# Kernel tuning notes

Measured on AMD Instinct MI355X. Metric: run time of the kernel, lower is better.

## Reference

```python
import jax, jax.numpy as jnp
import numpy as np

NUM_NODES = 116
EMBED = 64
HIDDEN = 64
OUT_FEAT = 116


def mish(x):
    return x * jnp.tanh(jax.nn.softplus(x))


def sage_conv(x, src, dst, w_l, b_l, w_r, n):
    # PyG SAGEConv (mean aggr): out = lin_l(mean_{j->i} x_j) + lin_r(x_i)
    agg = jax.ops.segment_sum(x[src], dst, num_segments=n)
    cnt = jax.ops.segment_sum(jnp.ones((src.shape[0],), x.dtype), dst, num_segments=n)
    mean = agg / jnp.clip(cnt, 1.0)[:, None]
    return mean @ w_l.T + b_l + x @ w_r.T


def setup_inputs() -> dict:
    key = jax.random.key(0)
    ks = jax.random.split(key, 12)
    B = 64
    N = B * NUM_NODES          # 7424 total nodes
    E = N * 32                 # 237568 edges
    d_in = EMBED * NUM_NODES   # 7424
    d_hid = HIDDEN * NUM_NODES # 7424
    d_out = OUT_FEAT * NUM_NODES  # 13456

    def lin_w(k, fan_out, fan_in):
        s = 1.0 / np.sqrt(fan_in)
        return jax.random.uniform(k, (fan_out, fan_in), jnp.float32, -s, s)

    return {
        "z": jax.random.normal(ks[0], (N, EMBED), jnp.float32),
        "edge_index": jax.random.randint(ks[1], (2, E), 0, N, jnp.int64),
        "batch_size": B,
        "w1_l": lin_w(ks[2], EMBED, EMBED),
        "b1_l": jnp.zeros((EMBED,), jnp.float32),
        "w1_r": lin_w(ks[3], EMBED, EMBED),
        "w2_l": lin_w(ks[4], EMBED, EMBED),
        "b2_l": jnp.zeros((EMBED,), jnp.float32),
        "w2_r": lin_w(ks[5], EMBED, EMBED),
        "fc1_w": lin_w(ks[6], d_hid, d_in),
        "fc1_b": jax.random.uniform(ks[7], (d_hid,), jnp.float32, -1/np.sqrt(d_in), 1/np.sqrt(d_in)),
        "fc2_w": lin_w(ks[8], d_out, d_hid),
        "fc2_b": jax.random.uniform(ks[9], (d_out,), jnp.float32, -1/np.sqrt(d_hid), 1/np.sqrt(d_hid)),
    }


def reference(z, edge_index, batch_size, w1_l, b1_l, w1_r, w2_l, b2_l, w2_r,
              fc1_w, fc1_b, fc2_w, fc2_b):
    n = z.shape[0]
    src, dst = edge_index[0], edge_index[1]
    h = mish(sage_conv(z, src, dst, w1_l, b1_l, w1_r, n))
    h = mish(sage_conv(h, src, dst, w2_l, b2_l, w2_r, n))
    h_flat = h.reshape(batch_size, NUM_NODES * EMBED)
    hidden = mish(h_flat @ fc1_w.T + fc1_b)
    x_rec = (hidden @ fc2_w.T + fc2_b).reshape(batch_size, NUM_NODES, OUT_FEAT)
    # enforce symmetry, unit diagonal
    sym = 0.5 * (x_rec + jnp.swapaxes(x_rec, 1, 2))
    eye = jnp.eye(NUM_NODES, dtype=bool)[None]
    sym = jnp.where(eye, jnp.asarray(1.0, sym.dtype), sym)
    return sym.reshape(batch_size * NUM_NODES, OUT_FEAT)
```

## Files before the change

kernel.cpp:

```cpp
#include <hip/hip_runtime.h>
#include <math.h>

#define NODES_TOT 7424
#define EDGES     237568
#define BATCH     64
#define NN        116
#define KDIM      7424
#define N1        7424
#define N2        13456
#define NKB       116
#define KSPLIT    8

typedef __attribute__((ext_vector_type(8))) short bf16x8;
typedef __attribute__((ext_vector_type(4))) float f32x4;
typedef __attribute__((ext_vector_type(4))) short s16x4;

__device__ __forceinline__ float mish_f(float v) {
    float sp = fmaxf(v, 0.0f) + log1pf(expf(-fabsf(v)));
    return v * tanhf(sp);
}

__device__ __forceinline__ unsigned short bf_rne(float f) {
    unsigned u = __float_as_uint(f);
    u += 0x7fffu + ((u >> 16) & 1u);
    return (unsigned short)(u >> 16);
}

__global__ void zero_kernel(int* __restrict__ p, int n) {
    int i = blockIdx.x * 256 + threadIdx.x;
    if (i < n) p[i] = 0;
}

__global__ void hist_kernel(const int* __restrict__ dst, int* __restrict__ hist) {
    int e = blockIdx.x * 256 + threadIdx.x;
    if (e < EDGES) atomicAdd(&hist[dst[e]], 1);
}

__global__ void scan_kernel(const int* __restrict__ hist, int* __restrict__ row_start,
                            int* __restrict__ cursor) {
    __shared__ int s[1024];
    int t = threadIdx.x;
    int base = t * 8;
    int loc[8];
    int sum = 0;
    #pragma unroll
    for (int c = 0; c < 8; ++c) {
        int idx = base + c;
        int v = (idx < NODES_TOT) ? hist[idx] : 0;
        loc[c] = sum;
        sum += v;
    }
    s[t] = sum;
    __syncthreads();
    for (int off = 1; off < 1024; off <<= 1) {
        int v = (t >= off) ? s[t - off] : 0;
        __syncthreads();
        s[t] += v;
        __syncthreads();
    }
    int excl = s[t] - sum;
    #pragma unroll
    for (int c = 0; c < 8; ++c) {
        int idx = base + c;
        if (idx < NODES_TOT) {
            int r = excl + loc[c];
            row_start[idx] = r;
            cursor[idx] = r;
        }
    }
}

__global__ void csr_fill_kernel(const int* __restrict__ src, const int* __restrict__ dst,
                                int* __restrict__ cursor, int* __restrict__ csr_src) {
    int e = blockIdx.x * 256 + threadIdx.x;
    if (e < EDGES) {
        int p = atomicAdd(&cursor[dst[e]], 1);
        csr_src[p] = src[e];
    }
}

template <bool BF>
__global__ void __launch_bounds__(256) conv_kernel(
        const float* __restrict__ x, const int* __restrict__ csr_src,
        const int* __restrict__ row_start, const int* __restrict__ deg_arr,
        const float* __restrict__ w_l, const float* __restrict__ b_l,
        const float* __restrict__ w_r, void* __restrict__ h_out_v) {
    __shared__ float wlT[64 * 64];
    __shared__ float wrT[64 * 64];
    __shared__ float mv[4][64];
    __shared__ float xv[4][64];
    int t = threadIdx.x;
    for (int i = 0; i < 16; ++i) {
        int idx = t + i * 256;
        int f = idx >> 6, k = idx & 63;
        wlT[k * 64 + f] = w_l[idx];
        wrT[k * 64 + f] = w_r[idx];
    }
    int g = t >> 6, f = t & 63;
    __syncthreads();
    for (int nb = blockIdx.x * 4; nb < NODES_TOT; nb += gridDim.x * 4) {
        int node = nb + g;
        int deg = deg_arr[node];
        int rs = row_start[node];
        float sum = 0.f;
        for (int e = 0; e < deg; ++e) {
            int s = csr_src[rs + e];
            sum += x[s * 64 + f];
        }
        float mean = sum / (float)max(deg, 1);
        mv[g][f] = mean;
        xv[g][f] = x[node * 64 + f];
        __syncthreads();
        float o = b_l[f];
        #pragma unroll
        for (int k = 0; k < 64; ++k) {
            o = fmaf(mv[g][k], wlT[k * 64 + f], o);
            o = fmaf(xv[g][k], wrT[k * 64 + f], o);
        }
        float m = mish_f(o);
        if (BF) ((unsigned short*)h_out_v)[node * 64 + f] = bf_rne(m);
        else    ((float*)h_out_v)[node * 64 + f] = m;
        __syncthreads();
    }
}

template <int KSHIFT>
__global__ void __launch_bounds__(256) gemm_tile(
        const unsigned short* __restrict__ Abf, const float* __restrict__ W,
        float* __restrict__ Cp, int N) {
    __shared__ __align__(16) short Wsh[2][4096];
    __shared__ __align__(16) short Ash[2][4096];
    int t = threadIdx.x;
    int bx = blockIdx.x, by = blockIdx.y;
    int kb0 = (by * NKB) >> KSHIFT;
    int kb1 = ((by + 1) * NKB) >> KSHIFT;
    int S = kb1 - kb0;
    int n0 = bx * 64;
    int r = t >> 2, q = t & 3;
    int wr = n0 + r; if (wr >= N) wr = N - 1;
    const float*          wsrc = W   + (size_t)wr * KDIM + (size_t)kb0 * 64 + q * 4;
    const unsigned short* asrc = Abf + (size_t)r  * KDIM + (size_t)kb0 * 64 + q * 8;
    int fb = q >> 1, hf = q & 1;
    int wv = t >> 6, l = t & 63, l15 = l & 15, hi = l >> 4;
    f32x4 acc[4];
    #pragma unroll
    for (int g = 0; g < 4; ++g) acc[g] = (f32x4){0.f, 0.f, 0.f, 0.f};

    f32x4 wA0, wA1, wA2, wA3, wB0, wB1, wB2, wB3;
    bf16x8 aA0, aA1, aB0, aB1;

#define ISSUE(W0, W1, W2, W3, A0, A1, step) do {                          \
        size_t kk = (size_t)(step) * 64;                                  \
        W0 = *(const f32x4*)(wsrc + kk);                                  \
        W1 = *(const f32x4*)(wsrc + kk + 16);                             \
        W2 = *(const f32x4*)(wsrc + kk + 32);                             \
        W3 = *(const f32x4*)(wsrc + kk + 48);                             \
        A0 = *(const bf16x8*)(asrc + kk);                                 \
        A1 = *(const bf16x8*)(asrc + kk + 32);                            \
    } while (0)

#define CONVWRITE(W0, W1, W2, W3, A0, A1, b) do {                         \
        s16x4 cv0, cv1, cv2, cv3;                                         \
        _Pragma("unroll")                                                 \
        for (int j = 0; j < 4; ++j) {                                     \
            cv0[j] = (short)bf_rne(W0[j]);                                \
            cv1[j] = (short)bf_rne(W1[j]);                                \
            cv2[j] = (short)bf_rne(W2[j]);                                \
            cv3[j] = (short)bf_rne(W3[j]);                                \
        }                                                                 \
        *(s16x4*)&Wsh[b][((0 * 2 + fb) * 64 + r) * 8 + hf * 4] = cv0;     \
        *(s16x4*)&Wsh[b][((1 * 2 + fb) * 64 + r) * 8 + hf * 4] = cv1;     \
        *(s16x4*)&Wsh[b][((2 * 2 + fb) * 64 + r) * 8 + hf * 4] = cv2;     \
        *(s16x4*)&Wsh[b][((3 * 2 + fb) * 64 + r) * 8 + hf * 4] = cv3;     \
        *(bf16x8*)&Ash[b][(q * 64 + r) * 8] = A0;                         \
        *(bf16x8*)&Ash[b][((q + 4) * 64 + r) * 8] = A1;                   \
    } while (0)

#define MFMAPH(b) do {                                                    \
        _Pragma("unroll")                                                 \
        for (int s = 0; s < 2; ++s) {                                     \
            int fw = s * 4 + hi;                                          \
            bf16x8 bh = *(const bf16x8*)&Wsh[b][(fw * 64 + wv * 16 + l15) * 8]; \
            _Pragma("unroll")                                             \
            for (int g = 0; g < 4; ++g) {                                 \
                bf16x8 av = *(const bf16x8*)&Ash[b][(fw * 64 + g * 16 + l15) * 8]; \
                acc[g] = __builtin_amdgcn_mfma_f32_16x16x32_bf16(av, bh, acc[g], 0, 0, 0); \
            }                                                             \
        }                                                                 \
    } while (0)

#define BAR() asm volatile("s_waitcnt lgkmcnt(0)\n\ts_barrier" ::: "memory")

    ISSUE(wA0, wA1, wA2, wA3, aA0, aA1, 0);
    ISSUE(wB0, wB1, wB2, wB3, aB0, aB1, 1);
    CONVWRITE(wA0, wA1, wA2, wA3, aA0, aA1, 0);
    BAR();

    int i = 0;
    for (; i + 1 < S - 1; i += 2) {
        if (i + 2 < S) ISSUE(wA0, wA1, wA2, wA3, aA0, aA1, i + 2);
        MFMAPH(0);
        CONVWRITE(wB0, wB1, wB2, wB3, aB0, aB1, 1);
        BAR();
        if (i + 3 < S) ISSUE(wB0, wB1, wB2, wB3, aB0, aB1, i + 3);
        MFMAPH(1);
        CONVWRITE(wA0, wA1, wA2, wA3, aA0, aA1, 0);
        BAR();
    }
    if (i < S - 1) {
        MFMAPH(0);
        CONVWRITE(wB0, wB1, wB2, wB3, aB0, aB1, 1);
        BAR();
        MFMAPH(1);
    } else {
        MFMAPH(0);
    }

#undef ISSUE
#undef CONVWRITE
#undef MFMAPH
#undef BAR

    int gn = n0 + wv * 16 + l15;
    if (gn < N) {
        float* cp = Cp + (size_t)by * 64 * N;
        #pragma unroll
        for (int g = 0; g < 4; ++g)
            #pragma unroll
            for (int rr = 0; rr < 4; ++rr)
                cp[(size_t)(g * 16 + hi * 4 + rr) * N + gn] = acc[g][rr];
    }
}

__global__ void reduce1_kernel(const float* __restrict__ Cp, const float* __restrict__ b,
                               unsigned short* __restrict__ A2) {
    int i4 = (blockIdx.x * 256 + threadIdx.x) * 4;
    if (i4 >= BATCH * N1) return;
    int n = i4 % N1;
    f32x4 acc = *(const f32x4*)(b + n);
    #pragma unroll
    for (int s = 0; s < KSPLIT; ++s)
        acc += *(const f32x4*)(Cp + (size_t)s * BATCH * N1 + i4);
    s16x4 o;
    #pragma unroll
    for (int j = 0; j < 4; ++j) o[j] = (short)bf_rne(mish_f(acc[j]));
    *(s16x4*)(A2 + i4) = o;
}

__global__ void reduce2_kernel(const float* __restrict__ Cp, const float* __restrict__ b,
                               float* __restrict__ C2) {
    int i4 = (blockIdx.x * 256 + threadIdx.x) * 4;
    if (i4 >= BATCH * N2) return;
    int n = i4 % N2;
    f32x4 acc = *(const f32x4*)(b + n);
    #pragma unroll
    for (int s = 0; s < KSPLIT; ++s)
        acc += *(const f32x4*)(Cp + (size_t)s * BATCH * N2 + i4);
    *(f32x4*)(C2 + i4) = acc;
}

__global__ void sym_kernel(const float* __restrict__ C2, float* __restrict__ out) {
    int tid = blockIdx.x * 256 + threadIdx.x;
    if (tid >= BATCH * NN * NN) return;
    int j = tid % NN;
    int r = tid / NN;
    int i = r % NN;
    int b = r / NN;
    float v;
    if (i == j) {
        v = 1.0f;
    } else {
        v = 0.5f * (C2[(size_t)b * N2 + i * NN + j] + C2[(size_t)b * N2 + j * NN + i]);
    }
    out[tid] = v;
}

extern "C" void kernel_launch(void* const* d_in, const int* in_sizes, int n_in,
                              void* d_out, int out_size, void* d_ws, size_t ws_size,
                              hipStream_t stream) {
    const float* z     = (const float*)d_in[0];
    const int*   edge  = (const int*)d_in[1];
    const float* w1_l  = (const float*)d_in[3];
    const float* b1_l  = (const float*)d_in[4];
    const float* w1_r  = (const float*)d_in[5];
    const float* w2_l  = (const float*)d_in[6];
    const float* b2_l  = (const float*)d_in[7];
    const float* w2_r  = (const float*)d_in[8];
    const float* fc1_w = (const float*)d_in[9];
    const float* fc1_b = (const float*)d_in[10];
    const float* fc2_w = (const float*)d_in[11];
    const float* fc2_b = (const float*)d_in[12];
    float* out = (float*)d_out;

    char* ws = (char*)d_ws;
    size_t off = 0;
    auto alloc = [&](size_t bytes) {
        void* p = ws + off;
        off = (off + bytes + 255) & ~(size_t)255;
        return p;
    };
    int*            hist      = (int*)alloc(NODES_TOT * 4);
    int*            row_start = (int*)alloc(NODES_TOT * 4);
    int*            cursor    = (int*)alloc(NODES_TOT * 4);
    int*            csr_src   = (int*)alloc((size_t)EDGES * 4);
    float*          h1        = (float*)alloc((size_t)NODES_TOT * 64 * 4);
    unsigned short* A1        = (unsigned short*)alloc((size_t)NODES_TOT * 64 * 2);
    float*          Cp1       = (float*)alloc((size_t)KSPLIT * BATCH * N1 * 4);
    unsigned short* A2        = (unsigned short*)alloc((size_t)BATCH * N1 * 2);
    float*          Cp2       = (float*)alloc((size_t)KSPLIT * BATCH * N2 * 4);
    float*          C2        = (float*)alloc((size_t)BATCH * N2 * 4);

    const int* src = edge;
    const int* dst = edge + EDGES;

    zero_kernel<<<(NODES_TOT + 255) / 256, 256, 0, stream>>>(hist, NODES_TOT);
    hist_kernel<<<(EDGES + 255) / 256, 256, 0, stream>>>(dst, hist);
    scan_kernel<<<1, 1024, 0, stream>>>(hist, row_start, cursor);
    csr_fill_kernel<<<(EDGES + 255) / 256, 256, 0, stream>>>(src, dst, cursor, csr_src);

    conv_kernel<false><<<928, 256, 0, stream>>>(z, csr_src, row_start, hist, w1_l, b1_l, w1_r, h1);
    conv_kernel<true><<<928, 256, 0, stream>>>(h1, csr_src, row_start, hist, w2_l, b2_l, w2_r, A1);

    gemm_tile<3><<<dim3(N1 / 64, KSPLIT), 256, 0, stream>>>(A1, fc1_w, Cp1, N1);
    reduce1_kernel<<<(BATCH * N1 / 4 + 255) / 256, 256, 0, stream>>>(Cp1, fc1_b, A2);

    gemm_tile<3><<<dim3((N2 + 63) / 64, KSPLIT), 256, 0, stream>>>(A2, fc2_w, Cp2, N2);
    reduce2_kernel<<<(BATCH * N2 / 4 + 255) / 256, 256, 0, stream>>>(Cp2, fc2_b, C2);

    sym_kernel<<<(BATCH * NN * NN + 255) / 256, 256, 0, stream>>>(C2, out);
}
```

Measured before the change: 324.4 us.

## Halve GEMM K-split and load weight rows in two-step bursts

The split-K factor for both FC GEMMs drops from 8 to 4, and each block now walks a fixed 29 k-blocks. Weight loads are issued in 128-element bursts covering two k-steps, so each thread issues wider contiguous reads further ahead of the MFMA phases. This halves the partial-sum traffic written and reduced, but launches half as many blocks and holds more loaded data in registers. The result could be lower occupancy or too few blocks to keep the GPU's compute units busy.

```diff
diff --git a/kernel.cpp b/kernel.cpp
--- a/kernel.cpp
+++ b/kernel.cpp
@@ -8,8 +8,7 @@
 #define KDIM      7424
 #define N1        7424
 #define N2        13456
-#define NKB       116
-#define KSPLIT    8
+#define KSPLIT    4
 
 typedef __attribute__((ext_vector_type(8))) short bf16x8;
 typedef __attribute__((ext_vector_type(4))) float f32x4;
@@ -124,42 +123,51 @@
     }
 }
 
-template <int KSHIFT>
-__global__ void __launch_bounds__(256) gemm_tile(
+__global__ void __launch_bounds__(256) gemm_burst(
         const unsigned short* __restrict__ Abf, const float* __restrict__ W,
         float* __restrict__ Cp, int N) {
     __shared__ __align__(16) short Wsh[2][4096];
     __shared__ __align__(16) short Ash[2][4096];
     int t = threadIdx.x;
     int bx = blockIdx.x, by = blockIdx.y;
-    int kb0 = (by * NKB) >> KSHIFT;
-    int kb1 = ((by + 1) * NKB) >> KSHIFT;
-    int S = kb1 - kb0;
     int n0 = bx * 64;
     int r = t >> 2, q = t & 3;
     int wr = n0 + r; if (wr >= N) wr = N - 1;
-    const float*          wsrc = W   + (size_t)wr * KDIM + (size_t)kb0 * 64 + q * 4;
-    const unsigned short* asrc = Abf + (size_t)r  * KDIM + (size_t)kb0 * 64 + q * 8;
+    const float*          wsrc = W   + (size_t)wr * KDIM + (size_t)by * 29 * 64 + q * 4;
+    const unsigned short* asrc = Abf + (size_t)r  * KDIM + (size_t)by * 29 * 64 + q * 8;
     int fb = q >> 1, hf = q & 1;
     int wv = t >> 6, l = t & 63, l15 = l & 15, hi = l >> 4;
     f32x4 acc[4];
     #pragma unroll
     for (int g = 0; g < 4; ++g) acc[g] = (f32x4){0.f, 0.f, 0.f, 0.f};
 
-    f32x4 wA0, wA1, wA2, wA3, wB0, wB1, wB2, wB3;
-    bf16x8 aA0, aA1, aB0, aB1;
-
-#define ISSUE(W0, W1, W2, W3, A0, A1, step) do {                          \
-        size_t kk = (size_t)(step) * 64;                                  \
-        W0 = *(const f32x4*)(wsrc + kk);                                  \
-        W1 = *(const f32x4*)(wsrc + kk + 16);                             \
-        W2 = *(const f32x4*)(wsrc + kk + 32);                             \
-        W3 = *(const f32x4*)(wsrc + kk + 48);                             \
-        A0 = *(const bf16x8*)(asrc + kk);                                 \
-        A1 = *(const bf16x8*)(asrc + kk + 32);                            \
-    } while (0)
-
-#define CONVWRITE(W0, W1, W2, W3, A0, A1, b) do {                         \
+    f32x4 wA[8], wB[8];
+    bf16x8 aEv[2], aOd[2];
+
+#define IW2(dst, s) do {                                                  \
+        dst[0] = *(const f32x4*)(wsrc + (s) * 64 + 0);                    \
+        dst[1] = *(const f32x4*)(wsrc + (s) * 64 + 16);                   \
+        dst[2] = *(const f32x4*)(wsrc + (s) * 64 + 32);                   \
+        dst[3] = *(const f32x4*)(wsrc + (s) * 64 + 48);                   \
+        dst[4] = *(const f32x4*)(wsrc + (s) * 64 + 64);                   \
+        dst[5] = *(const f32x4*)(wsrc + (s) * 64 + 80);                   \
+        dst[6] = *(const f32x4*)(wsrc + (s) * 64 + 96);                   \
+        dst[7] = *(const f32x4*)(wsrc + (s) * 64 + 112);                  \
+    } while (0)
+
+#define IW1(dst, s) do {                                                  \
+        dst[0] = *(const f32x4*)(wsrc + (s) * 64 + 0);                    \
+        dst[1] = *(const f32x4*)(wsrc + (s) * 64 + 16);                   \
+        dst[2] = *(const f32x4*)(wsrc + (s) * 64 + 32);                   \
+        dst[3] = *(const f32x4*)(wsrc + (s) * 64 + 48);                   \
+    } while (0)
+
+#define IA(dst, s) do {                                                   \
+        dst[0] = *(const bf16x8*)(asrc + (s) * 64);                       \
+        dst[1] = *(const bf16x8*)(asrc + (s) * 64 + 32);                  \
+    } while (0)
+
+#define CW(W0, W1, W2, W3, av, b) do {                                    \
         s16x4 cv0, cv1, cv2, cv3;                                         \
         _Pragma("unroll")                                                 \
         for (int j = 0; j < 4; ++j) {                                     \
@@ -168,12 +176,12 @@
             cv2[j] = (short)bf_rne(W2[j]);                                \
             cv3[j] = (short)bf_rne(W3[j]);                                \
         }                                                                 \
-        *(s16x4*)&Wsh[b][((0 * 2 + fb) * 64 + r) * 8 + hf * 4] = cv0;     \
-        *(s16x4*)&Wsh[b][((1 * 2 + fb) * 64 + r) * 8 + hf * 4] = cv1;     \
-        *(s16x4*)&Wsh[b][((2 * 2 + fb) * 64 + r) * 8 + hf * 4] = cv2;     \
-        *(s16x4*)&Wsh[b][((3 * 2 + fb) * 64 + r) * 8 + hf * 4] = cv3;     \
-        *(bf16x8*)&Ash[b][(q * 64 + r) * 8] = A0;                         \
-        *(bf16x8*)&Ash[b][((q + 4) * 64 + r) * 8] = A1;                   \
+        *(s16x4*)&Wsh[b][((0 + fb) * 64 + r) * 8 + hf * 4] = cv0;         \
+        *(s16x4*)&Wsh[b][((2 + fb) * 64 + r) * 8 + hf * 4] = cv1;         \
+        *(s16x4*)&Wsh[b][((4 + fb) * 64 + r) * 8 + hf * 4] = cv2;         \
+        *(s16x4*)&Wsh[b][((6 + fb) * 64 + r) * 8 + hf * 4] = cv3;         \
+        *(bf16x8*)&Ash[b][(q * 64 + r) * 8] = av[0];                      \
+        *(bf16x8*)&Ash[b][((q + 4) * 64 + r) * 8] = av[1];                \
     } while (0)
 
 #define MFMAPH(b) do {                                                    \
@@ -183,43 +191,50 @@
             bf16x8 bh = *(const bf16x8*)&Wsh[b][(fw * 64 + wv * 16 + l15) * 8]; \
             _Pragma("unroll")                                             \
             for (int g = 0; g < 4; ++g) {                                 \
-                bf16x8 av = *(const bf16x8*)&Ash[b][(fw * 64 + g * 16 + l15) * 8]; \
-                acc[g] = __builtin_amdgcn_mfma_f32_16x16x32_bf16(av, bh, acc[g], 0, 0, 0); \
+                bf16x8 avv = *(const bf16x8*)&Ash[b][(fw * 64 + g * 16 + l15) * 8]; \
+                acc[g] = __builtin_amdgcn_mfma_f32_16x16x32_bf16(avv, bh, acc[g], 0, 0, 0); \
             }                                                             \
         }                                                                 \
     } while (0)
 
-#define BAR() asm volatile("s_waitcnt lgkmcnt(0)\n\ts_barrier" ::: "memory")
-
-    ISSUE(wA0, wA1, wA2, wA3, aA0, aA1, 0);
-    ISSUE(wB0, wB1, wB2, wB3, aB0, aB1, 1);
-    CONVWRITE(wA0, wA1, wA2, wA3, aA0, aA1, 0);
-    BAR();
-
-    int i = 0;
-    for (; i + 1 < S - 1; i += 2) {
-        if (i + 2 < S) ISSUE(wA0, wA1, wA2, wA3, aA0, aA1, i + 2);
+#define LBAR() asm volatile("s_waitcnt lgkmcnt(0)\n\ts_barrier" ::: "memory")
+
+    IW2(wA, 0);
+    IW2(wB, 2);
+    IA(aEv, 0);
+    IA(aOd, 1);
+    CW(wA[0], wA[1], wA[2], wA[3], aEv, 0);
+    LBAR();
+
+    for (int g = 0; g < 7; ++g) {
+        int kb = g * 4;
         MFMAPH(0);
-        CONVWRITE(wB0, wB1, wB2, wB3, aB0, aB1, 1);
-        BAR();
-        if (i + 3 < S) ISSUE(wB0, wB1, wB2, wB3, aB0, aB1, i + 3);
+        CW(wA[4], wA[5], wA[6], wA[7], aOd, 1);
+        IA(aEv, kb + 2);
+        LBAR();
+        if (g < 6) IW2(wA, kb + 4); else IW1(wA, 28);
         MFMAPH(1);
-        CONVWRITE(wA0, wA1, wA2, wA3, aA0, aA1, 0);
-        BAR();
-    }
-    if (i < S - 1) {
+        CW(wB[0], wB[1], wB[2], wB[3], aEv, 0);
+        IA(aOd, kb + 3);
+        LBAR();
         MFMAPH(0);
-        CONVWRITE(wB0, wB1, wB2, wB3, aB0, aB1, 1);
-        BAR();
+        CW(wB[4], wB[5], wB[6], wB[7], aOd, 1);
+        IA(aEv, kb + 4);
+        LBAR();
+        if (g < 6) IW2(wB, kb + 6);
         MFMAPH(1);
-    } else {
-        MFMAPH(0);
-    }
-
-#undef ISSUE
-#undef CONVWRITE
+        CW(wA[0], wA[1], wA[2], wA[3], aEv, 0);
+        if (g < 6) IA(aOd, kb + 5);
+        LBAR();
+    }
+    MFMAPH(0);
+
+#undef IW2
+#undef IW1
+#undef IA
+#undef CW
 #undef MFMAPH
-#undef BAR
+#undef LBAR
 
     int gn = n0 + wv * 16 + l15;
     if (gn < N) {
@@ -321,10 +336,10 @@
     conv_kernel<false><<<928, 256, 0, stream>>>(z, csr_src, row_start, hist, w1_l, b1_l, w1_r, h1);
     conv_kernel<true><<<928, 256, 0, stream>>>(h1, csr_src, row_start, hist, w2_l, b2_l, w2_r, A1);
 
-    gemm_tile<3><<<dim3(N1 / 64, KSPLIT), 256, 0, stream>>>(A1, fc1_w, Cp1, N1);
+    gemm_burst<<<dim3(N1 / 64, KSPLIT), 256, 0, stream>>>(A1, fc1_w, Cp1, N1);
     reduce1_kernel<<<(BATCH * N1 / 4 + 255) / 256, 256, 0, stream>>>(Cp1, fc1_b, A2);
 
-    gemm_tile<3><<<dim3((N2 + 63) / 64, KSPLIT), 256, 0, stream>>>(A2, fc2_w, Cp2, N2);
+    gemm_burst<<<dim3((N2 + 63) / 64, KSPLIT), 256, 0, stream>>>(A2, fc2_w, Cp2, N2);
     reduce2_kernel<<<(BATCH * N2 / 4 + 255) / 256, 256, 0, stream>>>(Cp2, fc2_b, C2);
 
     sym_kernel<<<(BATCH * NN * NN + 255) / 256, 256, 0, stream>>>(C2, out);
```

Measured after the change: 317.0 us, median of 2. -2.3%, faster.
